# Kernel tuning notes

Hardware: AMD Instinct MI355X
Metric: run time of the kernel (lower is better)

Reference implementation:

```python
import jax, jax.numpy as jnp
import numpy as np

B, S, V, E, R1, R2, L = 16, 128, 32000, 128, 256, 640, 512


def pos_encoding(seq_len, d, n=10000.0):
    # P[k, 2i] = sin(k / n^(2i/d)); P[k, 2i+1] = cos(k / n^(2i/d))
    k = jnp.arange(seq_len, dtype=jnp.float32)[:, None]
    i = jnp.arange(d // 2, dtype=jnp.float32)[None, :]
    ang = k / jnp.power(jnp.float32(n), 2.0 * i / d)
    P = jnp.zeros((seq_len, d), dtype=jnp.float32)
    P = P.at[:, 0::2].set(jnp.sin(ang)).at[:, 1::2].set(jnp.cos(ang))
    return P


def setup_inputs() -> dict:
    key = jax.random.key(0)
    ks = iter(jax.random.split(key, 40))

    def lin(fin, fout):
        W = jax.random.normal(next(ks), (fin, fout), jnp.float32) / np.sqrt(fin)
        b = jax.random.normal(next(ks), (fout,), jnp.float32) * 0.01
        return W, b

    inp = {}
    inp['x'] = jax.random.normal(next(ks), (B, S, V), jnp.float32)
    inp['W_emb'], inp['b_emb'] = lin(V, E)
    inp['W_pos1'], inp['b_pos1'] = lin(2 * E, E)
    inp['W_red'], inp['b_red'] = lin(S * E, R1)
    inp['W_pos2'], inp['b_pos2'] = lin(2 * R1, R1)
    inp['W_red2'], inp['b_red2'] = lin(S * R1, R2)
    inp['W_pos3'], inp['b_pos3'] = lin(2 * R2, R2)
    inp['W_down2'], inp['b_down2'] = lin(R2, L)
    inp['W_flat'], inp['b_flat'] = lin(L * S, L)
    inp['W_d1'], inp['b_d1'] = lin(L, L)
    inp['W_d2'], inp['b_d2'] = lin(L, L)
    inp['W_d3'], inp['b_d3'] = lin(L, L)
    inp['W_p1'], inp['b_p1'] = lin(L, V)
    inp['W_p2'], inp['b_p2'] = lin(L, V)
    return inp


def _square_memory(h):
    # einsum('bij,bkm->bikj') factorizes: out[b,i,k,j] = h[b,i,j] * sum_m h[b,k,m]
    b, s, d = h.shape
    row_sum = h.sum(axis=-1)                       # (B, S)
    q = h[:, :, None, :] * row_sum[:, None, :, None]  # (B, S, S, D)
    return q.reshape(b, s, s * d)


def reference(x, W_emb, b_emb, W_pos1, b_pos1, W_red, b_red, W_pos2, b_pos2,
              W_red2, b_red2, W_pos3, b_pos3, W_down2, b_down2, W_flat, b_flat,
              W_d1, b_d1, W_d2, b_d2, W_d3, b_d3, W_p1, b_p1, W_p2, b_p2):
    relu = jax.nn.relu
    h = relu(x @ W_emb + b_emb)                                  # (B,S,E)
    h = h + relu(pos_encoding(S, 2 * E) @ W_pos1 + b_pos1)
    h = relu(_square_memory(h) @ W_red + b_red)                  # (B,S,R1)
    h = h + relu(pos_encoding(S, 2 * R1) @ W_pos2 + b_pos2)
    h = relu(_square_memory(h) @ W_red2 + b_red2)                # (B,S,R2)
    h = h + relu(pos_encoding(S, 2 * R2) @ W_pos3 + b_pos3)
    h = relu(h @ W_down2 + b_down2)                              # (B,S,L)
    h = relu(h.reshape(h.shape[0], -1) @ W_flat + b_flat)        # (B,L)
    h = relu(h @ W_d1 + b_d1)
    p1 = h @ W_p1 + b_p1
    h = relu(h @ W_d2 + b_d2)
    p2 = h @ W_p2 + b_p2
    h = relu(h @ W_d3 + b_d3)
    p3 = h @ W_p1 + b_p1  # faithful to source: project_1 reused (project_3 unused)
    return p1 + p2 + p3
```

## Files before the change

### kernel.cpp

```cpp
#include <hip/hip_runtime.h>

typedef float  f4   __attribute__((ext_vector_type(4)));
typedef __bf16 bf8_t __attribute__((ext_vector_type(8)));
typedef __bf16 bf4_t __attribute__((ext_vector_type(4)));

__device__ __forceinline__ void glds16(const void* g, void* l) {
    __builtin_amdgcn_global_load_lds(
        (const __attribute__((address_space(1))) void*)g,
        (__attribute__((address_space(3))) void*)l, 16, 0, 0);
}

__global__ __launch_bounds__(256)
void pos_enc_kernel(float* __restrict__ P1, float* __restrict__ P2,
                    float* __restrict__ P3,
                    const float* __restrict__ bp1, const float* __restrict__ bp2,
                    float* __restrict__ bc) {
    int idx = blockIdx.x * 256 + threadIdx.x;
    const int n1 = 128 * 256, n2 = 128 * 512, n3 = 128 * 1280;
    const int nP = n1 + n2 + n3;
    if (idx >= nP) {
        int j = idx - nP;
        if (j < 32000) bc[j] = 2.f * bp1[j] + bp2[j];
        return;
    }
    float* P; int d, local;
    if (idx < n1)           { P = P1; d = 256;  local = idx; }
    else if (idx < n1 + n2) { P = P2; d = 512;  local = idx - n1; }
    else                    { P = P3; d = 1280; local = idx - n1 - n2; }
    int s = local / d;
    int k = local - s * d;
    int i = k >> 1;
    float expo = (-2.0f * (float)i) / (float)d;
    float ang  = (float)s * powf(10000.0f, expo);
    P[local] = (k & 1) ? cosf(ang) : sinf(ang);
}

__global__ __launch_bounds__(256)
void transpose_bf16_k(const float* __restrict__ Wemb, __bf16* __restrict__ WembT,
                      const float* __restrict__ Wd2, __bf16* __restrict__ Wd2T,
                      const float* __restrict__ Wq1, __bf16* __restrict__ Wq1T,
                      const float* __restrict__ Wq2, __bf16* __restrict__ Wq2T,
                      const float* __restrict__ Wq3, __bf16* __restrict__ Wq3T) {
    const int bid = blockIdx.x;
    const float* src; __bf16* dst; int CN, RK, tn, local;
    if (bid < 4000)      { src = Wemb; dst = WembT; RK = 32000; CN = 128; tn = 4;  local = bid; }
    else if (bid < 4320) { src = Wd2;  dst = Wd2T;  RK = 640;   CN = 512; tn = 16; local = bid - 4000; }
    else if (bid < 4352) { src = Wq1;  dst = Wq1T;  RK = 256;   CN = 128; tn = 4;  local = bid - 4320; }
    else if (bid < 4480) { src = Wq2;  dst = Wq2T;  RK = 512;   CN = 256; tn = 8;  local = bid - 4352; }
    else                 { src = Wq3;  dst = Wq3T;  RK = 1280;  CN = 640; tn = 20; local = bid - 4480; }
    const int kt = local / tn, ntl = local - kt * tn;
    const int k0 = kt * 32, n0 = ntl * 32;
    __shared__ float tile[32][33];
    const int t = threadIdx.x;
    const int r = t >> 3, c4 = (t & 7) * 4;
    const f4 v = *(const f4*)(src + (long)(k0 + r) * CN + n0 + c4);
    tile[r][c4] = v[0]; tile[r][c4 + 1] = v[1];
    tile[r][c4 + 2] = v[2]; tile[r][c4 + 3] = v[3];
    __syncthreads();
    bf4_t o2;
    o2[0] = (__bf16)tile[c4][r];     o2[1] = (__bf16)tile[c4 + 1][r];
    o2[2] = (__bf16)tile[c4 + 2][r]; o2[3] = (__bf16)tile[c4 + 3][r];
    *(bf4_t*)(dst + (long)(n0 + r) * RK + k0 + c4) = o2;
}

template<int BMODE>
__global__ __launch_bounds__(256)
void gemm_v2(const float* __restrict__ A, const void* __restrict__ Bv,
             float* __restrict__ C, const float* __restrict__ bias,
             const float* __restrict__ addsrc,
             int M, int N, int K, int lda, int ldb, int ldc,
             long sA, long sB, long sC, int ksplit, int kchunk, int relu,
             int xcdmap) {
    __shared__ __align__(16) float AsF[2][2048];
    __shared__ __align__(16) float Bbuf[2][BMODE ? 4096 : 2048];

    const int t = threadIdx.x;
    int bn, bm, bz;
    if (xcdmap) {
        const int lin = blockIdx.x;
        const int xc = lin & 7, j = lin >> 3;
        bz = xc + ((j >> 5) << 3);
        bm = j & 31;
        bn = 0;
    } else { bn = blockIdx.x; bm = blockIdx.y; bz = blockIdx.z; }
    const int batch = bz / ksplit;
    const int kz = bz - batch * ksplit;
    const int m0 = bm * 64, n0 = bn * 128;
    const int kb = kz * kchunk;
    const int ke = (kb + kchunk < K) ? (kb + kchunk) : K;
    const int nit = (ke - kb + 31) >> 5;

    const int lane = t & 63;
    const int w = t >> 6;
    const int wm = w >> 1, wn = w & 1;
    const int fr = lane & 15;
    const int fq = (lane >> 4) * 8;

    f4 acc[2][4];
#pragma unroll
    for (int mt = 0; mt < 2; ++mt)
#pragma unroll
        for (int nt = 0; nt < 4; ++nt) acc[mt][nt] = (f4){0.f, 0.f, 0.f, 0.f};

    const float* Ab = A + (long)batch * sA;
    const int mvalid = M - m0;

    const int ra = t >> 3;
    const int ja = (t & 7) ^ (ra & 7);
    const float* aS0 = Ab + (long)(m0 + ra) * lda + 4 * ja;
    const float* aS1 = aS0 + 32L * lda;

    const __bf16* bTS0 = nullptr; const __bf16* bTS1 = nullptr;
    const float* bNS0 = nullptr;
    if constexpr (BMODE == 0) {
        const __bf16* BT = (const __bf16*)Bv + (long)batch * sB;
        const int nb = t >> 2;
        const int fb = (nb & 3) ^ ((nb >> 2) & 3);
        const int jb = (t & 3) ^ fb;
        bTS0 = BT + (long)(n0 + nb) * ldb + 8 * jb;
        bTS1 = bTS0 + 64L * ldb;
    } else {
        const float* Bn = (const float*)Bv + (long)batch * sB;
        bNS0 = Bn + (long)(t >> 5) * ldb + n0 + (t & 31) * 4;
    }

    auto STAGE = [&](int b, int k0) {
        if (ra < mvalid)      glds16(aS0 + k0, AsF[b] + 4 * t);
        if (ra + 32 < mvalid) glds16(aS1 + k0, AsF[b] + 1024 + 4 * t);
        if constexpr (BMODE == 0) {
            glds16(bTS0 + k0, Bbuf[b] + 4 * t);
            glds16(bTS1 + k0, Bbuf[b] + 1024 + 4 * t);
        } else {
            const float* bp = bNS0 + (long)k0 * ldb;
            glds16(bp,             Bbuf[b] + 4 * t);
            glds16(bp + 8L * ldb,  Bbuf[b] + 1024 + 4 * t);
            glds16(bp + 16L * ldb, Bbuf[b] + 2048 + 4 * t);
            glds16(bp + 24L * ldb, Bbuf[b] + 3072 + 4 * t);
        }
    };

    const int R0 = wm * 32 + fr, R1 = R0 + 16;
    const int jq = (lane >> 4) * 2;
    const int x7 = R0 & 7;
    const int aO00 = R0 * 8 + (jq ^ x7);
    const int aO01 = R0 * 8 + ((jq + 1) ^ x7);
    const int aO10 = R1 * 8 + (jq ^ x7);
    const int aO11 = R1 * 8 + ((jq + 1) ^ x7);
    int bOf[4];
    if constexpr (BMODE == 0) {
        const int fbc = (fr & 3) ^ ((fr >> 2) & 3);
        const int jb2 = (lane >> 4) ^ fbc;
#pragma unroll
        for (int nt = 0; nt < 4; ++nt)
            bOf[nt] = ((wn * 64 + nt * 16 + fr) * 4 + jb2) * 8;
    } else {
#pragma unroll
        for (int nt = 0; nt < 4; ++nt)
            bOf[nt] = wn * 64 + nt * 16 + fr;
    }

    STAGE(0, kb);
    __syncthreads();
    int cur = 0;
    for (int i = 0; i < nit; ++i) {
        if (i + 1 < nit) STAGE(cur ^ 1, kb + (i + 1) * 32);

        const float* Ac = AsF[cur];
        f4 x0 = *(const f4*)(Ac + aO00 * 4);
        f4 x1 = *(const f4*)(Ac + aO01 * 4);
        f4 x2 = *(const f4*)(Ac + aO10 * 4);
        f4 x3 = *(const f4*)(Ac + aO11 * 4);
        bf8_t af0, af1;
#pragma unroll
        for (int q = 0; q < 4; ++q) {
            af0[q] = (__bf16)x0[q]; af0[4 + q] = (__bf16)x1[q];
            af1[q] = (__bf16)x2[q]; af1[4 + q] = (__bf16)x3[q];
        }
#pragma unroll
        for (int nt = 0; nt < 4; ++nt) {
            bf8_t bv;
            if constexpr (BMODE == 0) {
                bv = *(const bf8_t*)((const __bf16*)Bbuf[cur] + bOf[nt]);
            } else {
                const float* bb = Bbuf[cur] + fq * 128 + bOf[nt];
#pragma unroll
                for (int d = 0; d < 8; ++d) bv[d] = (__bf16)bb[d * 128];
            }
            acc[0][nt] = __builtin_amdgcn_mfma_f32_16x16x32_bf16(af0, bv, acc[0][nt], 0, 0, 0);
            acc[1][nt] = __builtin_amdgcn_mfma_f32_16x16x32_bf16(af1, bv, acc[1][nt], 0, 0, 0);
        }
        __syncthreads();
        cur ^= 1;
    }

    float* Cp; long ldcp;
    const bool fin = (ksplit == 1);
    if (!fin) { Cp = C + (long)(batch * ksplit + kz) * M * N; ldcp = N; }
    else      { Cp = C + (long)batch * sC;                    ldcp = ldc; }

    const int rb = m0 + wm * 32 + (lane >> 4) * 4;
    const int cb_ = n0 + wn * 64 + fr;
#pragma unroll
    for (int mt = 0; mt < 2; ++mt) {
#pragma unroll
        for (int nt = 0; nt < 4; ++nt) {
            const int c = cb_ + nt * 16;
            const float bvl = (fin && bias) ? bias[c] : 0.f;
#pragma unroll
            for (int v = 0; v < 4; ++v) {
                const int r = rb + mt * 16 + v;
                if (r < M) {
                    float val = acc[mt][nt][v] + bvl;
                    if (fin && relu) val = fmaxf(val, 0.f);
                    if (fin && addsrc) val += addsrc[(long)r * ldcp + c];
                    Cp[(long)r * ldcp + c] = val;
                }
            }
        }
    }
}

__global__ __launch_bounds__(256)
void reduce_splitk(const float* __restrict__ part, float* __restrict__ outp,
                   const float* __restrict__ bias, int MN, int N, int ksplit,
                   int relu) {
    int idx = blockIdx.x * 256 + threadIdx.x;
    if (idx >= MN) return;
    float s = 0.f;
    for (int z = 0; z < ksplit; ++z) s += part[(long)z * MN + idx];
    if (bias) s += bias[idx % N];
    if (relu) s = fmaxf(s, 0.f);
    outp[idx] = s;
}

__global__ __launch_bounds__(256)
void reduce_rs_kernel(const float* __restrict__ part, float* __restrict__ h1,
                      const float* __restrict__ bias, const float* __restrict__ Q1,
                      float* __restrict__ rs1, int ksplit) {
    const int t = threadIdx.x;
    const int idx = blockIdx.x * 256 + t;
    float s = 0.f;
    for (int z = 0; z < ksplit; ++z) s += part[(long)z * 262144 + idx];
    s += bias[idx & 127];
    s = fmaxf(s, 0.f);
    s += Q1[idx & 16383];
    h1[idx] = s;
    float r = s;
    for (int off = 32; off > 0; off >>= 1) r += __shfl_down(r, off, 64);
    __shared__ float p[4];
    const int w = t >> 6, lane = t & 63;
    if (lane == 0) p[w] = r;
    __syncthreads();
    if (t < 2) rs1[(blockIdx.x << 1) + t] = p[t * 2] + p[t * 2 + 1];
}

__global__ __launch_bounds__(256)
void rowsum_kernel(const float* __restrict__ h, float* __restrict__ rs,
                   int rows, int D) {
    int gw = (blockIdx.x * 256 + threadIdx.x) >> 6;
    int lane = threadIdx.x & 63;
    if (gw >= rows) return;
    const float* p = h + (long)gw * D;
    float s = 0.f;
    for (int j = lane; j < D; j += 64) s += p[j];
    for (int off = 32; off > 0; off >>= 1) s += __shfl_down(s, off, 64);
    if (lane == 0) rs[gw] = s;
}

extern "C" void kernel_launch(void* const* d_in, const int* in_sizes, int n_in,
                              void* d_out, int out_size, void* d_ws, size_t ws_size,
                              hipStream_t stream) {
    const float* x       = (const float*)d_in[0];
    const float* W_emb   = (const float*)d_in[1];
    const float* b_emb   = (const float*)d_in[2];
    const float* W_pos1  = (const float*)d_in[3];
    const float* b_pos1  = (const float*)d_in[4];
    const float* W_red   = (const float*)d_in[5];
    const float* b_red   = (const float*)d_in[6];
    const float* W_pos2  = (const float*)d_in[7];
    const float* b_pos2  = (const float*)d_in[8];
    const float* W_red2  = (const float*)d_in[9];
    const float* b_red2  = (const float*)d_in[10];
    const float* W_pos3  = (const float*)d_in[11];
    const float* b_pos3  = (const float*)d_in[12];
    const float* W_down2 = (const float*)d_in[13];
    const float* b_down2 = (const float*)d_in[14];
    const float* W_flat  = (const float*)d_in[15];
    const float* b_flat  = (const float*)d_in[16];
    const float* W_d1    = (const float*)d_in[17];
    const float* b_d1    = (const float*)d_in[18];
    const float* W_d2    = (const float*)d_in[19];
    const float* b_d2    = (const float*)d_in[20];
    const float* W_d3    = (const float*)d_in[21];
    const float* b_d3    = (const float*)d_in[22];
    const float* W_p1    = (const float*)d_in[23];
    const float* b_p1    = (const float*)d_in[24];
    const float* W_p2    = (const float*)d_in[25];
    const float* b_p2    = (const float*)d_in[26];
    float* out = (float*)d_out;
    float* ws  = (float*)d_ws;

    size_t o = 0;
    auto alloc = [&](size_t n) { size_t p = o; o += (n + 63) & ~(size_t)63; return p; };
    const size_t oP1 = alloc(128 * 256);
    const size_t oP2 = alloc(128 * 512);
    const size_t oP3 = alloc(128 * 1280);
    const size_t oQ1 = alloc(128 * 128);
    const size_t oQ2 = alloc(128 * 256);
    const size_t oQ3 = alloc(128 * 640);
    const size_t oBC = alloc(32000);
    const size_t oH1 = alloc(2048 * 128);
    const size_t oRS1 = alloc(2048);
    const size_t oRS2 = alloc(2048);
    const size_t oH2 = alloc(2048 * 256);
    const size_t oH3 = alloc(2048 * 640);
    const size_t oH4 = alloc(2048 * 512);
    const size_t oH5 = alloc(16 * 512);
    const size_t oH6 = alloc(16 * 512);
    const size_t oH7 = alloc(16 * 512);
    const size_t oH8 = alloc(16 * 512);
    const size_t oM1 = alloc(16 * 32768);
    const size_t oM2 = alloc(16 * 163840);
    const size_t oWembT = alloc(2048000);
    const size_t oWd2T  = alloc(163840);
    const size_t oQ1T   = alloc(16384);
    const size_t oQ2T   = alloc(65536);
    const size_t oQ3T   = alloc(409600);
    const size_t oRegA = alloc(32u * 262144);
    const size_t oPartQ3 = oRegA, oPartG1 = oRegA, oPartF = oRegA;
    (void)ws_size; (void)in_sizes; (void)n_in; (void)out_size;

    __bf16* WembT = (__bf16*)(ws + oWembT);
    __bf16* Wd2T  = (__bf16*)(ws + oWd2T);
    __bf16* Q1T   = (__bf16*)(ws + oQ1T);
    __bf16* Q2T   = (__bf16*)(ws + oQ2T);
    __bf16* Q3T   = (__bf16*)(ws + oQ3T);

    dim3 blk(256);

    pos_enc_kernel<<<dim3(1149), blk, 0, stream>>>(ws + oP1, ws + oP2, ws + oP3,
                                                   b_p1, b_p2, ws + oBC);
    transpose_bf16_k<<<dim3(5280), blk, 0, stream>>>(W_emb, WembT, W_down2, Wd2T,
                                                     W_pos1, Q1T, W_pos2, Q2T,
                                                     W_pos3, Q3T);
    gemm_v2<0><<<dim3(1, 2, 1), blk, 0, stream>>>(ws + oP1, Q1T, ws + oQ1,
        b_pos1, nullptr, 128, 128, 256, 256, 256, 128, 0, 0, 0, 1, 256, 1, 0);
    gemm_v2<0><<<dim3(2, 2, 1), blk, 0, stream>>>(ws + oP2, Q2T, ws + oQ2,
        b_pos2, nullptr, 128, 256, 512, 512, 512, 256, 0, 0, 0, 1, 512, 1, 0);
    gemm_v2<0><<<dim3(5, 2, 4), blk, 0, stream>>>(ws + oP3, Q3T, ws + oPartQ3,
        nullptr, nullptr, 128, 640, 1280, 1280, 1280, 640, 0, 0, 0, 4, 320, 0, 0);
    reduce_splitk<<<dim3(320), blk, 0, stream>>>(ws + oPartQ3, ws + oQ3, b_pos3,
                                                 81920, 640, 4, 1);
    gemm_v2<0><<<dim3(1024), blk, 0, stream>>>(x, WembT, ws + oPartG1,
        nullptr, nullptr, 2048, 128, 32000, 32000, 32000, 128, 0, 0, 0, 32, 1024, 0, 1);
    reduce_rs_kernel<<<dim3(1024), blk, 0, stream>>>(ws + oPartG1, ws + oH1, b_emb,
                                                     ws + oQ1, ws + oRS1, 32);
    gemm_v2<1><<<dim3(256, 1, 1), blk, 0, stream>>>(ws + oRS1, W_red, ws + oM1,
        nullptr, nullptr, 16, 32768, 128, 128, 32768, 32768, 0, 0, 0, 1, 128, 0, 0);
    gemm_v2<1><<<dim3(2, 2, 16), blk, 0, stream>>>(ws + oH1, ws + oM1, ws + oH2,
        b_red, ws + oQ2, 128, 256, 128, 128, 256, 256, 16384, 32768, 32768, 1, 128, 1, 0);
    rowsum_kernel<<<dim3(512), blk, 0, stream>>>(ws + oH2, ws + oRS2, 2048, 256);
    gemm_v2<1><<<dim3(1280, 1, 1), blk, 0, stream>>>(ws + oRS2, W_red2, ws + oM2,
        nullptr, nullptr, 16, 163840, 128, 128, 163840, 163840, 0, 0, 0, 1, 128, 0, 0);
    gemm_v2<1><<<dim3(5, 2, 16), blk, 0, stream>>>(ws + oH2, ws + oM2, ws + oH3,
        b_red2, ws + oQ3, 128, 640, 256, 256, 640, 640, 32768, 163840, 81920, 1, 256, 1, 0);
    gemm_v2<0><<<dim3(4, 32, 1), blk, 0, stream>>>(ws + oH3, Wd2T, ws + oH4,
        b_down2, nullptr, 2048, 512, 640, 640, 640, 512, 0, 0, 0, 1, 640, 1, 0);
    gemm_v2<1><<<dim3(4, 1, 64), blk, 0, stream>>>(ws + oH4, W_flat, ws + oPartF,
        nullptr, nullptr, 16, 512, 65536, 65536, 512, 512, 0, 0, 0, 64, 1024, 0, 0);
    reduce_splitk<<<dim3(32), blk, 0, stream>>>(ws + oPartF, ws + oH5, b_flat,
                                                8192, 512, 64, 1);
    gemm_v2<1><<<dim3(4, 1, 1), blk, 0, stream>>>(ws + oH5, W_d1, ws + oH6,
        b_d1, nullptr, 16, 512, 512, 512, 512, 512, 0, 0, 0, 1, 512, 1, 0);
    gemm_v2<1><<<dim3(4, 1, 1), blk, 0, stream>>>(ws + oH6, W_d2, ws + oH7,
        b_d2, nullptr, 16, 512, 512, 512, 512, 512, 0, 0, 0, 1, 512, 1, 0);
    gemm_v2<1><<<dim3(4, 1, 1), blk, 0, stream>>>(ws + oH7, W_d3, ws + oH8,
        b_d3, ws + oH6, 16, 512, 512, 512, 512, 512, 0, 0, 0, 1, 512, 1, 0);
    gemm_v2<1><<<dim3(250, 1, 1), blk, 0, stream>>>(ws + oH8, W_p1, out,
        ws + oBC, nullptr, 16, 32000, 512, 512, 32000, 32000, 0, 0, 0, 1, 512, 0, 0);
    gemm_v2<1><<<dim3(250, 1, 1), blk, 0, stream>>>(ws + oH7, W_p2, out,
        nullptr, out, 16, 32000, 512, 512, 32000, 32000, 0, 0, 0, 1, 512, 0, 0);
}
```

Before: 448.1 us.

## Fuse prep kernels, merge pos-encoding GEMMs into embedding launch, fuse rowsum and projections

Merges the positional-encoding and transpose kernels into a single prep kernel. The three positional GEMMs now run as extra blocks inside the embedding GEMM launch, which removes the split-K for pos3 and its reduction. The layer-2 row sum is computed in the GEMM epilogue with atomics, so the separate rowsum kernel goes away. The two final 32000-wide projections become one K=1024 GEMM that switches B source at k=512 over concatenated activations. Together these cut the launch count and one full re-read of the output, at the cost of atomics and of running the pos3 GEMM unsplit in a single block along K.

```diff
diff --git a/kernel.cpp b/kernel.cpp
--- a/kernel.cpp
+++ b/kernel.cpp
@@ -11,78 +11,71 @@
 }
 
 __global__ __launch_bounds__(256)
-void pos_enc_kernel(float* __restrict__ P1, float* __restrict__ P2,
-                    float* __restrict__ P3,
-                    const float* __restrict__ bp1, const float* __restrict__ bp2,
-                    float* __restrict__ bc) {
-    int idx = blockIdx.x * 256 + threadIdx.x;
-    const int n1 = 128 * 256, n2 = 128 * 512, n3 = 128 * 1280;
-    const int nP = n1 + n2 + n3;
-    if (idx >= nP) {
+void prep_kernel(float* __restrict__ P1, float* __restrict__ P2,
+                 float* __restrict__ P3,
+                 const float* __restrict__ bp1, const float* __restrict__ bp2,
+                 float* __restrict__ bc, float* __restrict__ rs2,
+                 const float* __restrict__ Wemb, __bf16* __restrict__ WembT,
+                 const float* __restrict__ Wd2, __bf16* __restrict__ Wd2T,
+                 const float* __restrict__ Wq1, __bf16* __restrict__ Wq1T,
+                 const float* __restrict__ Wq2, __bf16* __restrict__ Wq2T,
+                 const float* __restrict__ Wq3, __bf16* __restrict__ Wq3T) {
+    const int bid = blockIdx.x;
+    const int t = threadIdx.x;
+    if (bid < 5280) {
+        const float* src; __bf16* dst; int CN, RK, tn, local;
+        if (bid < 4000)      { src = Wemb; dst = WembT; RK = 32000; CN = 128; tn = 4;  local = bid; }
+        else if (bid < 4320) { src = Wd2;  dst = Wd2T;  RK = 640;   CN = 512; tn = 16; local = bid - 4000; }
+        else if (bid < 4352) { src = Wq1;  dst = Wq1T;  RK = 256;   CN = 128; tn = 4;  local = bid - 4320; }
+        else if (bid < 4480) { src = Wq2;  dst = Wq2T;  RK = 512;   CN = 256; tn = 8;  local = bid - 4352; }
+        else                 { src = Wq3;  dst = Wq3T;  RK = 1280;  CN = 640; tn = 20; local = bid - 4480; }
+        const int kt = local / tn, ntl = local - kt * tn;
+        const int k0 = kt * 32, n0 = ntl * 32;
+        __shared__ float tile[32][33];
+        const int r = t >> 3, c4 = (t & 7) * 4;
+        const f4 v = *(const f4*)(src + (long)(k0 + r) * CN + n0 + c4);
+        tile[r][c4] = v[0]; tile[r][c4 + 1] = v[1];
+        tile[r][c4 + 2] = v[2]; tile[r][c4 + 3] = v[3];
+        __syncthreads();
+        bf4_t o2;
+        o2[0] = (__bf16)tile[c4][r];     o2[1] = (__bf16)tile[c4 + 1][r];
+        o2[2] = (__bf16)tile[c4 + 2][r]; o2[3] = (__bf16)tile[c4 + 3][r];
+        *(bf4_t*)(dst + (long)(n0 + r) * RK + k0 + c4) = o2;
+        return;
+    }
+    int idx = (bid - 5280) * 256 + t;
+    const int n1 = 128 * 256, n2 = 128 * 512;
+    const int nP = 262144;
+    if (idx < nP) {
+        float* P; int d, local;
+        if (idx < n1)           { P = P1; d = 256;  local = idx; }
+        else if (idx < n1 + n2) { P = P2; d = 512;  local = idx - n1; }
+        else                    { P = P3; d = 1280; local = idx - n1 - n2; }
+        int s = local / d;
+        int k = local - s * d;
+        int i = k >> 1;
+        float ang = (float)s * powf(10000.0f, (-2.0f * (float)i) / (float)d);
+        P[local] = (k & 1) ? cosf(ang) : sinf(ang);
+    } else if (idx < nP + 32000) {
         int j = idx - nP;
-        if (j < 32000) bc[j] = 2.f * bp1[j] + bp2[j];
-        return;
-    }
-    float* P; int d, local;
-    if (idx < n1)           { P = P1; d = 256;  local = idx; }
-    else if (idx < n1 + n2) { P = P2; d = 512;  local = idx - n1; }
-    else                    { P = P3; d = 1280; local = idx - n1 - n2; }
-    int s = local / d;
-    int k = local - s * d;
-    int i = k >> 1;
-    float expo = (-2.0f * (float)i) / (float)d;
-    float ang  = (float)s * powf(10000.0f, expo);
-    P[local] = (k & 1) ? cosf(ang) : sinf(ang);
-}
-
-__global__ __launch_bounds__(256)
-void transpose_bf16_k(const float* __restrict__ Wemb, __bf16* __restrict__ WembT,
-                      const float* __restrict__ Wd2, __bf16* __restrict__ Wd2T,
-                      const float* __restrict__ Wq1, __bf16* __restrict__ Wq1T,
-                      const float* __restrict__ Wq2, __bf16* __restrict__ Wq2T,
-                      const float* __restrict__ Wq3, __bf16* __restrict__ Wq3T) {
-    const int bid = blockIdx.x;
-    const float* src; __bf16* dst; int CN, RK, tn, local;
-    if (bid < 4000)      { src = Wemb; dst = WembT; RK = 32000; CN = 128; tn = 4;  local = bid; }
-    else if (bid < 4320) { src = Wd2;  dst = Wd2T;  RK = 640;   CN = 512; tn = 16; local = bid - 4000; }
-    else if (bid < 4352) { src = Wq1;  dst = Wq1T;  RK = 256;   CN = 128; tn = 4;  local = bid - 4320; }
-    else if (bid < 4480) { src = Wq2;  dst = Wq2T;  RK = 512;   CN = 256; tn = 8;  local = bid - 4352; }
-    else                 { src = Wq3;  dst = Wq3T;  RK = 1280;  CN = 640; tn = 20; local = bid - 4480; }
-    const int kt = local / tn, ntl = local - kt * tn;
-    const int k0 = kt * 32, n0 = ntl * 32;
-    __shared__ float tile[32][33];
+        bc[j] = 2.f * bp1[j] + bp2[j];
+    } else if (idx < nP + 32000 + 2048) {
+        rs2[idx - nP - 32000] = 0.f;
+    }
+}
+
+template<int BMODE>
+__device__ __forceinline__ void gemm_dev(
+    float* As0, float* As1, float* Bb0, float* Bb1,
+    const float* __restrict__ A, const void* __restrict__ Bv,
+    const void* __restrict__ B2v, float* __restrict__ C,
+    const float* __restrict__ bias, const float* __restrict__ addsrc,
+    float* __restrict__ rsum,
+    int M, int N, int K, int lda, int ldb, int ldc, int kswitch,
+    long sA, long sB, long sC, int ksplit, int kchunk, int relu,
+    int bn, int bm, int bz) {
+
     const int t = threadIdx.x;
-    const int r = t >> 3, c4 = (t & 7) * 4;
-    const f4 v = *(const f4*)(src + (long)(k0 + r) * CN + n0 + c4);
-    tile[r][c4] = v[0]; tile[r][c4 + 1] = v[1];
-    tile[r][c4 + 2] = v[2]; tile[r][c4 + 3] = v[3];
-    __syncthreads();
-    bf4_t o2;
-    o2[0] = (__bf16)tile[c4][r];     o2[1] = (__bf16)tile[c4 + 1][r];
-    o2[2] = (__bf16)tile[c4 + 2][r]; o2[3] = (__bf16)tile[c4 + 3][r];
-    *(bf4_t*)(dst + (long)(n0 + r) * RK + k0 + c4) = o2;
-}
-
-template<int BMODE>
-__global__ __launch_bounds__(256)
-void gemm_v2(const float* __restrict__ A, const void* __restrict__ Bv,
-             float* __restrict__ C, const float* __restrict__ bias,
-             const float* __restrict__ addsrc,
-             int M, int N, int K, int lda, int ldb, int ldc,
-             long sA, long sB, long sC, int ksplit, int kchunk, int relu,
-             int xcdmap) {
-    __shared__ __align__(16) float AsF[2][2048];
-    __shared__ __align__(16) float Bbuf[2][BMODE ? 4096 : 2048];
-
-    const int t = threadIdx.x;
-    int bn, bm, bz;
-    if (xcdmap) {
-        const int lin = blockIdx.x;
-        const int xc = lin & 7, j = lin >> 3;
-        bz = xc + ((j >> 5) << 3);
-        bm = j & 31;
-        bn = 0;
-    } else { bn = blockIdx.x; bm = blockIdx.y; bz = blockIdx.z; }
     const int batch = bz / ksplit;
     const int kz = bz - batch * ksplit;
     const int m0 = bm * 64, n0 = bn * 128;
@@ -111,7 +104,7 @@
     const float* aS1 = aS0 + 32L * lda;
 
     const __bf16* bTS0 = nullptr; const __bf16* bTS1 = nullptr;
-    const float* bNS0 = nullptr;
+    const float* bNS0 = nullptr; const float* bNS2 = nullptr;
     if constexpr (BMODE == 0) {
         const __bf16* BT = (const __bf16*)Bv + (long)batch * sB;
         const int nb = t >> 2;
@@ -122,20 +115,23 @@
     } else {
         const float* Bn = (const float*)Bv + (long)batch * sB;
         bNS0 = Bn + (long)(t >> 5) * ldb + n0 + (t & 31) * 4;
-    }
-
-    auto STAGE = [&](int b, int k0) {
-        if (ra < mvalid)      glds16(aS0 + k0, AsF[b] + 4 * t);
-        if (ra + 32 < mvalid) glds16(aS1 + k0, AsF[b] + 1024 + 4 * t);
+        const float* Bn2 = (const float*)(B2v ? B2v : Bv);
+        bNS2 = Bn2 + (long)(t >> 5) * ldb + n0 + (t & 31) * 4;
+    }
+
+    auto STAGE = [&](float* Ad, float* Bd, int k0) {
+        if (ra < mvalid)      glds16(aS0 + k0, Ad + 4 * t);
+        if (ra + 32 < mvalid) glds16(aS1 + k0, Ad + 1024 + 4 * t);
         if constexpr (BMODE == 0) {
-            glds16(bTS0 + k0, Bbuf[b] + 4 * t);
-            glds16(bTS1 + k0, Bbuf[b] + 1024 + 4 * t);
+            glds16(bTS0 + k0, Bd + 4 * t);
+            glds16(bTS1 + k0, Bd + 1024 + 4 * t);
         } else {
-            const float* bp = bNS0 + (long)k0 * ldb;
-            glds16(bp,             Bbuf[b] + 4 * t);
-            glds16(bp + 8L * ldb,  Bbuf[b] + 1024 + 4 * t);
-            glds16(bp + 16L * ldb, Bbuf[b] + 2048 + 4 * t);
-            glds16(bp + 24L * ldb, Bbuf[b] + 3072 + 4 * t);
+            const float* bp = (k0 < kswitch) ? (bNS0 + (long)k0 * ldb)
+                                             : (bNS2 + (long)(k0 - kswitch) * ldb);
+            glds16(bp,             Bd + 4 * t);
+            glds16(bp + 8L * ldb,  Bd + 1024 + 4 * t);
+            glds16(bp + 16L * ldb, Bd + 2048 + 4 * t);
+            glds16(bp + 24L * ldb, Bd + 3072 + 4 * t);
         }
     };
 
@@ -159,13 +155,14 @@
             bOf[nt] = wn * 64 + nt * 16 + fr;
     }
 
-    STAGE(0, kb);
+    STAGE(As0, Bb0, kb);
     __syncthreads();
     int cur = 0;
     for (int i = 0; i < nit; ++i) {
-        if (i + 1 < nit) STAGE(cur ^ 1, kb + (i + 1) * 32);
-
-        const float* Ac = AsF[cur];
+        float* Ac = cur ? As1 : As0;
+        float* Bc = cur ? Bb1 : Bb0;
+        if (i + 1 < nit) STAGE(cur ? As0 : As1, cur ? Bb0 : Bb1, kb + (i + 1) * 32);
+
         f4 x0 = *(const f4*)(Ac + aO00 * 4);
         f4 x1 = *(const f4*)(Ac + aO01 * 4);
         f4 x2 = *(const f4*)(Ac + aO10 * 4);
@@ -180,9 +177,9 @@
         for (int nt = 0; nt < 4; ++nt) {
             bf8_t bv;
             if constexpr (BMODE == 0) {
-                bv = *(const bf8_t*)((const __bf16*)Bbuf[cur] + bOf[nt]);
+                bv = *(const bf8_t*)((const __bf16*)Bc + bOf[nt]);
             } else {
-                const float* bb = Bbuf[cur] + fq * 128 + bOf[nt];
+                const float* bb = Bc + fq * 128 + bOf[nt];
 #pragma unroll
                 for (int d = 0; d < 8; ++d) bv[d] = (__bf16)bb[d * 128];
             }
@@ -200,6 +197,7 @@
 
     const int rb = m0 + wm * 32 + (lane >> 4) * 4;
     const int cb_ = n0 + wn * 64 + fr;
+    float rowpart[2][4] = {{0.f,0.f,0.f,0.f},{0.f,0.f,0.f,0.f}};
 #pragma unroll
     for (int mt = 0; mt < 2; ++mt) {
 #pragma unroll
@@ -214,9 +212,80 @@
                     if (fin && relu) val = fmaxf(val, 0.f);
                     if (fin && addsrc) val += addsrc[(long)r * ldcp + c];
                     Cp[(long)r * ldcp + c] = val;
+                    rowpart[mt][v] += val;
                 }
             }
         }
+    }
+    if (rsum) {
+#pragma unroll
+        for (int mt = 0; mt < 2; ++mt) {
+#pragma unroll
+            for (int v = 0; v < 4; ++v) {
+                float s = rowpart[mt][v];
+                s += __shfl_xor(s, 1); s += __shfl_xor(s, 2);
+                s += __shfl_xor(s, 4); s += __shfl_xor(s, 8);
+                const int r = rb + mt * 16 + v;
+                if (fr == 0 && r < M) atomicAdd(&rsum[(long)bz * M + r], s);
+            }
+        }
+    }
+}
+
+template<int BMODE>
+__global__ __launch_bounds__(256)
+void gemm_v2(const float* A, const void* Bv, const void* B2v, float* C,
+             const float* bias, const float* addsrc, float* rsum,
+             int M, int N, int K, int lda, int ldb, int ldc, int kswitch,
+             long sA, long sB, long sC, int ksplit, int kchunk, int relu) {
+    __shared__ __align__(16) float AsF[2][2048];
+    __shared__ __align__(16) float Bbuf[2][BMODE ? 4096 : 2048];
+    gemm_dev<BMODE>(&AsF[0][0], &AsF[1][0], &Bbuf[0][0], &Bbuf[1][0],
+                    A, Bv, B2v, C, bias, addsrc, rsum,
+                    M, N, K, lda, ldb, ldc, kswitch, sA, sB, sC,
+                    ksplit, kchunk, relu,
+                    blockIdx.x, blockIdx.y, blockIdx.z);
+}
+
+__global__ __launch_bounds__(256)
+void mega1_kernel(const float* __restrict__ x, const __bf16* __restrict__ WembT,
+                  float* __restrict__ partG1,
+                  const float* __restrict__ P1, const __bf16* __restrict__ Q1T,
+                  float* __restrict__ Q1o, const float* __restrict__ bq1,
+                  const float* __restrict__ P2, const __bf16* __restrict__ Q2T,
+                  float* __restrict__ Q2o, const float* __restrict__ bq2,
+                  const float* __restrict__ P3, const __bf16* __restrict__ Q3T,
+                  float* __restrict__ Q3o, const float* __restrict__ bq3) {
+    __shared__ __align__(16) float AsF[2][2048];
+    __shared__ __align__(16) float Bbuf[2][2048];
+    float* A0 = &AsF[0][0]; float* A1 = &AsF[1][0];
+    float* B0 = &Bbuf[0][0]; float* B1 = &Bbuf[1][0];
+    const int bid = blockIdx.x;
+    if (bid < 1024) {
+        const int xc = bid & 7, j = bid >> 3;
+        const int bz = xc + ((j >> 5) << 3);
+        const int bm = j & 31;
+        gemm_dev<0>(A0, A1, B0, B1, x, WembT, nullptr, partG1,
+                    nullptr, nullptr, nullptr,
+                    2048, 128, 32000, 32000, 32000, 128, 32000,
+                    0, 0, 0, 32, 1024, 0, 0, bm, bz);
+    } else if (bid < 1026) {
+        gemm_dev<0>(A0, A1, B0, B1, P1, Q1T, nullptr, Q1o,
+                    bq1, nullptr, nullptr,
+                    128, 128, 256, 256, 256, 128, 256,
+                    0, 0, 0, 1, 256, 1, 0, bid - 1024, 0);
+    } else if (bid < 1030) {
+        const int l = bid - 1026;
+        gemm_dev<0>(A0, A1, B0, B1, P2, Q2T, nullptr, Q2o,
+                    bq2, nullptr, nullptr,
+                    128, 256, 512, 512, 512, 256, 512,
+                    0, 0, 0, 1, 512, 1, l & 1, l >> 1, 0);
+    } else {
+        const int l = bid - 1030;
+        gemm_dev<0>(A0, A1, B0, B1, P3, Q3T, nullptr, Q3o,
+                    bq3, nullptr, nullptr,
+                    128, 640, 1280, 1280, 1280, 640, 1280,
+                    0, 0, 0, 1, 1280, 1, l % 5, l / 5, 0);
     }
 }
 
@@ -252,19 +321,6 @@
     if (lane == 0) p[w] = r;
     __syncthreads();
     if (t < 2) rs1[(blockIdx.x << 1) + t] = p[t * 2] + p[t * 2 + 1];
-}
-
-__global__ __launch_bounds__(256)
-void rowsum_kernel(const float* __restrict__ h, float* __restrict__ rs,
-                   int rows, int D) {
-    int gw = (blockIdx.x * 256 + threadIdx.x) >> 6;
-    int lane = threadIdx.x & 63;
-    if (gw >= rows) return;
-    const float* p = h + (long)gw * D;
-    float s = 0.f;
-    for (int j = lane; j < D; j += 64) s += p[j];
-    for (int off = 32; off > 0; off >>= 1) s += __shfl_down(s, off, 64);
-    if (lane == 0) rs[gw] = s;
 }
 
 extern "C" void kernel_launch(void* const* d_in, const int* in_sizes, int n_in,
@@ -316,9 +372,8 @@
     const size_t oH3 = alloc(2048 * 640);
     const size_t oH4 = alloc(2048 * 512);
     const size_t oH5 = alloc(16 * 512);
-    const size_t oH6 = alloc(16 * 512);
-    const size_t oH7 = alloc(16 * 512);
-    const size_t oH8 = alloc(16 * 512);
+    const size_t oH6c = alloc(16 * 1024);
+    const size_t oCat = alloc(16 * 1024);
     const size_t oM1 = alloc(16 * 32768);
     const size_t oM2 = alloc(16 * 163840);
     const size_t oWembT = alloc(2048000);
@@ -327,7 +382,7 @@
     const size_t oQ2T   = alloc(65536);
     const size_t oQ3T   = alloc(409600);
     const size_t oRegA = alloc(32u * 262144);
-    const size_t oPartQ3 = oRegA, oPartG1 = oRegA, oPartF = oRegA;
+    const size_t oPartG1 = oRegA, oPartF = oRegA;
     (void)ws_size; (void)in_sizes; (void)n_in; (void)out_size;
 
     __bf16* WembT = (__bf16*)(ws + oWembT);
@@ -338,46 +393,46 @@
 
     dim3 blk(256);
 
-    pos_enc_kernel<<<dim3(1149), blk, 0, stream>>>(ws + oP1, ws + oP2, ws + oP3,
-                                                   b_p1, b_p2, ws + oBC);
-    transpose_bf16_k<<<dim3(5280), blk, 0, stream>>>(W_emb, WembT, W_down2, Wd2T,
-                                                     W_pos1, Q1T, W_pos2, Q2T,
-                                                     W_pos3, Q3T);
-    gemm_v2<0><<<dim3(1, 2, 1), blk, 0, stream>>>(ws + oP1, Q1T, ws + oQ1,
-        b_pos1, nullptr, 128, 128, 256, 256, 256, 128, 0, 0, 0, 1, 256, 1, 0);
-    gemm_v2<0><<<dim3(2, 2, 1), blk, 0, stream>>>(ws + oP2, Q2T, ws + oQ2,
-        b_pos2, nullptr, 128, 256, 512, 512, 512, 256, 0, 0, 0, 1, 512, 1, 0);
-    gemm_v2<0><<<dim3(5, 2, 4), blk, 0, stream>>>(ws + oP3, Q3T, ws + oPartQ3,
-        nullptr, nullptr, 128, 640, 1280, 1280, 1280, 640, 0, 0, 0, 4, 320, 0, 0);
-    reduce_splitk<<<dim3(320), blk, 0, stream>>>(ws + oPartQ3, ws + oQ3, b_pos3,
-                                                 81920, 640, 4, 1);
-    gemm_v2<0><<<dim3(1024), blk, 0, stream>>>(x, WembT, ws + oPartG1,
-        nullptr, nullptr, 2048, 128, 32000, 32000, 32000, 128, 0, 0, 0, 32, 1024, 0, 1);
-    reduce_rs_kernel<<<dim3(1024), blk, 0, stream>>>(ws + oPartG1, ws + oH1, b_emb,
-                                                     ws + oQ1, ws + oRS1, 32);
-    gemm_v2<1><<<dim3(256, 1, 1), blk, 0, stream>>>(ws + oRS1, W_red, ws + oM1,
-        nullptr, nullptr, 16, 32768, 128, 128, 32768, 32768, 0, 0, 0, 1, 128, 0, 0);
-    gemm_v2<1><<<dim3(2, 2, 16), blk, 0, stream>>>(ws + oH1, ws + oM1, ws + oH2,
-        b_red, ws + oQ2, 128, 256, 128, 128, 256, 256, 16384, 32768, 32768, 1, 128, 1, 0);
-    rowsum_kernel<<<dim3(512), blk, 0, stream>>>(ws + oH2, ws + oRS2, 2048, 256);
-    gemm_v2<1><<<dim3(1280, 1, 1), blk, 0, stream>>>(ws + oRS2, W_red2, ws + oM2,
-        nullptr, nullptr, 16, 163840, 128, 128, 163840, 163840, 0, 0, 0, 1, 128, 0, 0);
-    gemm_v2<1><<<dim3(5, 2, 16), blk, 0, stream>>>(ws + oH2, ws + oM2, ws + oH3,
-        b_red2, ws + oQ3, 128, 640, 256, 256, 640, 640, 32768, 163840, 81920, 1, 256, 1, 0);
-    gemm_v2<0><<<dim3(4, 32, 1), blk, 0, stream>>>(ws + oH3, Wd2T, ws + oH4,
-        b_down2, nullptr, 2048, 512, 640, 640, 640, 512, 0, 0, 0, 1, 640, 1, 0);
-    gemm_v2<1><<<dim3(4, 1, 64), blk, 0, stream>>>(ws + oH4, W_flat, ws + oPartF,
-        nullptr, nullptr, 16, 512, 65536, 65536, 512, 512, 0, 0, 0, 64, 1024, 0, 0);
+    prep_kernel<<<dim3(6437), blk, 0, stream>>>(
+        ws + oP1, ws + oP2, ws + oP3, b_p1, b_p2, ws + oBC, ws + oRS2,
+        W_emb, WembT, W_down2, Wd2T, W_pos1, Q1T, W_pos2, Q2T, W_pos3, Q3T);
+    mega1_kernel<<<dim3(1040), blk, 0, stream>>>(
+        x, WembT, ws + oPartG1,
+        ws + oP1, Q1T, ws + oQ1, b_pos1,
+        ws + oP2, Q2T, ws + oQ2, b_pos2,
+        ws + oP3, Q3T, ws + oQ3, b_pos3);
+    reduce_rs_kernel<<<dim3(1024), blk, 0, stream>>>(ws + oPartG1, ws + oH1,
+                                                     b_emb, ws + oQ1, ws + oRS1, 32);
+    gemm_v2<1><<<dim3(256, 1, 1), blk, 0, stream>>>(ws + oRS1, W_red, nullptr,
+        ws + oM1, nullptr, nullptr, nullptr,
+        16, 32768, 128, 128, 32768, 32768, 128, 0, 0, 0, 1, 128, 0);
+    gemm_v2<1><<<dim3(2, 2, 16), blk, 0, stream>>>(ws + oH1, ws + oM1, nullptr,
+        ws + oH2, b_red, ws + oQ2, ws + oRS2,
+        128, 256, 128, 128, 256, 256, 128, 16384, 32768, 32768, 1, 128, 1);
+    gemm_v2<1><<<dim3(1280, 1, 1), blk, 0, stream>>>(ws + oRS2, W_red2, nullptr,
+        ws + oM2, nullptr, nullptr, nullptr,
+        16, 163840, 128, 128, 163840, 163840, 128, 0, 0, 0, 1, 128, 0);
+    gemm_v2<1><<<dim3(5, 2, 16), blk, 0, stream>>>(ws + oH2, ws + oM2, nullptr,
+        ws + oH3, b_red2, ws + oQ3, nullptr,
+        128, 640, 256, 256, 640, 640, 256, 32768, 163840, 81920, 1, 256, 1);
+    gemm_v2<0><<<dim3(4, 32, 1), blk, 0, stream>>>(ws + oH3, Wd2T, nullptr,
+        ws + oH4, b_down2, nullptr, nullptr,
+        2048, 512, 640, 640, 640, 512, 640, 0, 0, 0, 1, 640, 1);
+    gemm_v2<1><<<dim3(4, 1, 64), blk, 0, stream>>>(ws + oH4, W_flat, nullptr,
+        ws + oPartF, nullptr, nullptr, nullptr,
+        16, 512, 65536, 65536, 512, 512, 65536, 0, 0, 0, 64, 1024, 0);
     reduce_splitk<<<dim3(32), blk, 0, stream>>>(ws + oPartF, ws + oH5, b_flat,
                                                 8192, 512, 64, 1);
-    gemm_v2<1><<<dim3(4, 1, 1), blk, 0, stream>>>(ws + oH5, W_d1, ws + oH6,
-        b_d1, nullptr, 16, 512, 512, 512, 512, 512, 0, 0, 0, 1, 512, 1, 0);
-    gemm_v2<1><<<dim3(4, 1, 1), blk, 0, stream>>>(ws + oH6, W_d2, ws + oH7,
-        b_d2, nullptr, 16, 512, 512, 512, 512, 512, 0, 0, 0, 1, 512, 1, 0);
-    gemm_v2<1><<<dim3(4, 1, 1), blk, 0, stream>>>(ws + oH7, W_d3, ws + oH8,
-        b_d3, ws + oH6, 16, 512, 512, 512, 512, 512, 0, 0, 0, 1, 512, 1, 0);
-    gemm_v2<1><<<dim3(250, 1, 1), blk, 0, stream>>>(ws + oH8, W_p1, out,
-        ws + oBC, nullptr, 16, 32000, 512, 512, 32000, 32000, 0, 0, 0, 1, 512, 0, 0);
-    gemm_v2<1><<<dim3(250, 1, 1), blk, 0, stream>>>(ws + oH7, W_p2, out,
-        nullptr, out, 16, 32000, 512, 512, 32000, 32000, 0, 0, 0, 1, 512, 0, 0);
-}
+    gemm_v2<1><<<dim3(4, 1, 1), blk, 0, stream>>>(ws + oH5, W_d1, nullptr,
+        ws + oH6c, b_d1, nullptr, nullptr,
+        16, 512, 512, 512, 512, 1024, 512, 0, 0, 0, 1, 512, 1);
+    gemm_v2<1><<<dim3(4, 1, 1), blk, 0, stream>>>(ws + oH6c, W_d2, nullptr,
+        ws + oCat + 512, b_d2, nullptr, nullptr,
+        16, 512, 512, 1024, 512, 1024, 512, 0, 0, 0, 1, 512, 1);
+    gemm_v2<1><<<dim3(4, 1, 1), blk, 0, stream>>>(ws + oCat + 512, W_d3, nullptr,
+        ws + oCat, b_d3, ws + oH6c, nullptr,
+        16, 512, 512, 1024, 512, 1024, 512, 0, 0, 0, 1, 512, 1);
+    gemm_v2<1><<<dim3(250, 1, 1), blk, 0, stream>>>(ws + oCat, W_p1, W_p2,
+        out, ws + oBC, nullptr, nullptr,
+        16, 32000, 1024, 1024, 32000, 32000, 512, 0, 0, 0, 1, 1024, 0);
+}
```

New measurement: 363.1 us. 1.23x faster.
